# Kernel tuning notes

Hardware: AMD Instinct MI355X
Metric: run time of the kernel (lower is better)

Reference implementation:

```python
import jax, jax.numpy as jnp
import numpy as np

NUM_HEADS = 16
EPS = 1e-6  # LinearAttention.epsilon

def setup_inputs() -> dict:
    key = jax.random.key(0)
    ks = jax.random.split(key, 10)
    B, L, D = 4, 4096, 2048
    s = 1.0 / np.sqrt(D)
    x = jax.random.normal(ks[0], (B, L, D), dtype=jnp.float32)
    attention_mask = jnp.ones((B, L), dtype=jnp.float32)
    Wq = jax.random.normal(ks[1], (D, D), dtype=jnp.float32) * s
    bq = jnp.zeros((D,), dtype=jnp.float32)
    Wk = jax.random.normal(ks[2], (D, D), dtype=jnp.float32) * s
    bk = jnp.zeros((D,), dtype=jnp.float32)
    Wv = jax.random.normal(ks[3], (D, D), dtype=jnp.float32) * s
    bv = jnp.zeros((D,), dtype=jnp.float32)
    Wo = jax.random.normal(ks[4], (D, D), dtype=jnp.float32) * s
    bo = jnp.zeros((D,), dtype=jnp.float32)
    return {"x": x, "attention_mask": attention_mask, "Wq": Wq, "bq": bq,
            "Wk": Wk, "bk": bk, "Wv": Wv, "bv": bv, "Wo": Wo, "bo": bo}

def reference(x, attention_mask, Wq, bq, Wk, bk, Wv, bv, Wo, bo):
    B, L, Dm = x.shape
    H = NUM_HEADS
    Dh = Dm // H
    # q/k/v projections -> [B, H, L, Dh]
    def proj(W, b):
        return (x @ W + b).reshape(B, L, H, Dh).transpose(0, 2, 1, 3)
    q = proj(Wq, bq)
    k = proj(Wk, bk)
    v = proj(Wv, bv)
    # feature map: elu(x) + 1
    q = jax.nn.elu(q) + 1.0
    k = jax.nn.elu(k) + 1.0
    # mask keys/values: mask [B, 1, L, 1]
    m = attention_mask[:, None, :, None]
    k = k * m
    v = v * m
    # causal linear attention via cumulative sums over sequence dim
    k_cum = jnp.cumsum(k, axis=2)          # [B,H,L,Dh]
    kv_cum = jnp.cumsum(k * v, axis=2)     # [B,H,L,Dh] (diagonal kv state, as in source)
    z = jnp.sum(q * k_cum, axis=-1) + EPS  # [B,H,L]
    z = z * attention_mask[:, None, :]
    out = (q * kv_cum) / z[..., None]      # [B,H,L,Dh]
    out = out.transpose(0, 2, 1, 3).reshape(B, L, Dm)
    return out @ Wo + bo
```

## Files before the change

### kernel.cpp

```cpp
#include <hip/hip_runtime.h>
#include <cstdint>
#include <cstddef>

#define EPS_F 1e-6f

__device__ inline unsigned short f2bf(float f) {
    union { float f; unsigned u; } v; v.f = f;
    unsigned r = v.u + 0x7fffu + ((v.u >> 16) & 1u);
    return (unsigned short)(r >> 16);
}
__device__ inline float bf2f(unsigned u16) {
    union { unsigned u; float f; } v; v.u = u16 << 16; return v.f;
}

typedef __attribute__((ext_vector_type(8))) __bf16 bf16x8;
typedef __attribute__((ext_vector_type(8))) short short8;
typedef __attribute__((ext_vector_type(8))) unsigned short ushort8;
typedef __attribute__((ext_vector_type(4))) float floatx4;

__device__ inline void async_load16(const void* g, void* l) {
    __builtin_amdgcn_global_load_lds((const __attribute__((address_space(1))) void*)g,
                                     (__attribute__((address_space(3))) void*)l,
                                     16, 0, 0);
}

__global__ void cast_x_kernel(const float* __restrict__ in, unsigned short* __restrict__ out, int n8) {
    int i = blockIdx.x * blockDim.x + threadIdx.x;
    if (i < n8) {
        float4 a = ((const float4*)in)[2 * i];
        float4 b = ((const float4*)in)[2 * i + 1];
        short8 o;
        o[0] = (short)f2bf(a.x); o[1] = (short)f2bf(a.y);
        o[2] = (short)f2bf(a.z); o[3] = (short)f2bf(a.w);
        o[4] = (short)f2bf(b.x); o[5] = (short)f2bf(b.y);
        o[6] = (short)f2bf(b.z); o[7] = (short)f2bf(b.w);
        ((short8*)out)[i] = o;
    }
}

__global__ void transpose_cast_kernel(const float* __restrict__ W0, const float* __restrict__ W1,
                                      const float* __restrict__ W2, const float* __restrict__ W3,
                                      unsigned short* __restrict__ WtBase, int n) {
    const float* W = (blockIdx.z == 0) ? W0 : (blockIdx.z == 1) ? W1 : (blockIdx.z == 2) ? W2 : W3;
    unsigned short* Wt = WtBase + (size_t)blockIdx.z * n * n;
    __shared__ float tile[32][33];
    int bx = blockIdx.x * 32;
    int by = blockIdx.y * 32;
    int tx = threadIdx.x;
    int ty = threadIdx.y;
    #pragma unroll
    for (int i = 0; i < 32; i += 8)
        tile[ty + i][tx] = W[(size_t)(by + ty + i) * n + bx + tx];
    __syncthreads();
    #pragma unroll
    for (int i = 0; i < 32; i += 8)
        Wt[(size_t)(bx + ty + i) * n + by + tx] = f2bf(tile[tx][ty + i]);
}

#define BMT 128
#define BNT 128
#define BKT 64
#define DMODEL 2048

template<int FINAL>
__global__ __launch_bounds__(256, 2)
void gemm_kernel(const unsigned short* __restrict__ A,
                 const unsigned short* __restrict__ Bt,
                 const float* __restrict__ b0, const float* __restrict__ b1,
                 const float* __restrict__ b2,
                 const float* __restrict__ mask,
                 unsigned short* __restrict__ qo, unsigned short* __restrict__ ko,
                 unsigned short* __restrict__ vo,
                 float* __restrict__ Cf,
                 int M, int K) {
    __shared__ __align__(16) unsigned short As[BMT * BKT];
    __shared__ __align__(16) unsigned short Bs[BNT * BKT];

    const int tid  = threadIdx.x;
    const int wave = tid >> 6;
    const int lane = tid & 63;
    const int m0    = blockIdx.x * BMT;
    const int nglob = blockIdx.y * BNT;
    int mat, n0;
    const float* bias;
    unsigned short* Cb = nullptr;
    if (FINAL) {
        mat = 0; n0 = nglob; bias = b0;
    } else {
        mat  = nglob >> 11;
        n0   = nglob & (DMODEL - 1);
        bias = (mat == 0) ? b0 : (mat == 1) ? b1 : b2;
        Cb   = (mat == 0) ? qo : (mat == 1) ? ko : vo;
    }
    const int wm = (wave >> 1) * 64;
    const int wn = (wave & 1) * 64;
    const int quad  = lane >> 4;
    const int row16 = lane & 15;

    floatx4 acc[4][4] = {};

    const int srow_lo = lane >> 3;
    const int schunk  = lane & 7;

    for (int k0 = 0; k0 < K; k0 += BKT) {
        #pragma unroll
        for (int i = 0; i < 4; i++) {
            int slot_base = wave * 256 + i * 64;
            int r  = wave * 32 + i * 8 + srow_lo;
            int cg = schunk ^ (r & 7);
            const unsigned short* ga = A  + (size_t)(m0 + r) * K + k0 + cg * 8;
            const unsigned short* gb = Bt + (size_t)(nglob + r) * K + k0 + cg * 8;
            async_load16(ga, As + (size_t)slot_base * 8);
            async_load16(gb, Bs + (size_t)slot_base * 8);
        }
        __syncthreads();

        #pragma unroll
        for (int kk = 0; kk < 2; kk++) {
            bf16x8 af[4], bfr[4];
            #pragma unroll
            for (int t = 0; t < 4; t++) {
                int ra = wm + t * 16 + row16;
                int ca = (kk * 4 + quad) ^ (ra & 7);
                af[t]  = __builtin_bit_cast(bf16x8, *(const short8*)(As + (size_t)ra * 64 + ca * 8));
                int rb = wn + t * 16 + row16;
                int cb = (kk * 4 + quad) ^ (rb & 7);
                bfr[t] = __builtin_bit_cast(bf16x8, *(const short8*)(Bs + (size_t)rb * 64 + cb * 8));
            }
            #pragma unroll
            for (int i = 0; i < 4; i++)
                #pragma unroll
                for (int j = 0; j < 4; j++)
                    acc[i][j] = __builtin_amdgcn_mfma_f32_16x16x32_bf16(af[i], bfr[j], acc[i][j], 0, 0, 0);
        }
        __syncthreads();
    }

    float bcache[4];
    #pragma unroll
    for (int j = 0; j < 4; j++) bcache[j] = bias[n0 + wn + j * 16 + row16];
    #pragma unroll
    for (int i = 0; i < 4; i++) {
        #pragma unroll
        for (int r = 0; r < 4; r++) {
            int row = m0 + wm + i * 16 + quad * 4 + r;
            float mr = 1.0f;
            if (!FINAL && mat >= 1) mr = mask[row];
            #pragma unroll
            for (int j = 0; j < 4; j++) {
                int col = n0 + wn + j * 16 + row16;
                float v = acc[i][j][r] + bcache[j];
                if (FINAL) {
                    Cf[(size_t)row * DMODEL + col] = v;
                } else {
                    if (mat <= 1) v = (v > 0.f) ? (v + 1.f) : __expf(v);
                    v *= mr;
                    Cb[(size_t)row * DMODEL + col] = f2bf(v);
                }
            }
        }
    }
}

#define SL    4096
#define SD    2048
#define SH    16
#define CHUNK 64
#define NCH   64

__global__ void scan_partial_kernel(const unsigned short* __restrict__ k,
                                    const unsigned short* __restrict__ v,
                                    float* __restrict__ sumK, float* __restrict__ sumKV) {
    int blk = blockIdx.x;
    int c = blk & (NCH - 1), bh = blk >> 6;
    int b = bh >> 4, h = bh & (SH - 1);
    int lane = threadIdx.x;
    int tg = lane >> 4, dg = lane & 15;
    size_t base = ((size_t)(b * SL + c * CHUNK + tg)) * SD + h * 128 + dg * 8;
    float sk[8] = {0.f, 0.f, 0.f, 0.f, 0.f, 0.f, 0.f, 0.f};
    float skv[8] = {0.f, 0.f, 0.f, 0.f, 0.f, 0.f, 0.f, 0.f};
    for (int it = 0; it < CHUNK / 4; it++) {
        ushort8 kw = *(const ushort8*)(k + base);
        ushort8 vw = *(const ushort8*)(v + base);
        #pragma unroll
        for (int j = 0; j < 8; j++) {
            float kf = bf2f(kw[j]);
            float vf = bf2f(vw[j]);
            sk[j] += kf; skv[j] += kf * vf;
        }
        base += (size_t)4 * SD;
    }
    #pragma unroll
    for (int j = 0; j < 8; j++) {
        sk[j]  += __shfl_xor(sk[j], 16);  sk[j]  += __shfl_xor(sk[j], 32);
        skv[j] += __shfl_xor(skv[j], 16); skv[j] += __shfl_xor(skv[j], 32);
    }
    if (tg == 0) {
        size_t o = ((size_t)bh * NCH + c) * 128 + dg * 8;
        *(float4*)(sumK  + o)     = make_float4(sk[0], sk[1], sk[2], sk[3]);
        *(float4*)(sumK  + o + 4) = make_float4(sk[4], sk[5], sk[6], sk[7]);
        *(float4*)(sumKV + o)     = make_float4(skv[0], skv[1], skv[2], skv[3]);
        *(float4*)(sumKV + o + 4) = make_float4(skv[4], skv[5], skv[6], skv[7]);
    }
}

__global__ void scan_offsets_kernel(const float* __restrict__ sumK, const float* __restrict__ sumKV,
                                    float* __restrict__ offK, float* __restrict__ offKV) {
    int bh = blockIdx.x;
    int d  = threadIdx.x;
    float aK = 0.f, aKV = 0.f;
    for (int c = 0; c < NCH; c++) {
        size_t o = ((size_t)bh * NCH + c) * 128 + d;
        float sk = sumK[o], skv = sumKV[o];
        offK[o] = aK; offKV[o] = aKV;
        aK += sk; aKV += skv;
    }
}

__global__ void scan_final_kernel(const unsigned short* __restrict__ q,
                                  const unsigned short* __restrict__ k,
                                  const unsigned short* __restrict__ v,
                                  const float* __restrict__ offK, const float* __restrict__ offKV,
                                  const float* __restrict__ mask,
                                  unsigned short* __restrict__ out) {
    int blk = blockIdx.x;
    int c = blk & (NCH - 1), bh = blk >> 6;
    int b = bh >> 4, h = bh & (SH - 1);
    int lane = threadIdx.x;
    size_t ob = ((size_t)bh * NCH + c) * 128 + 2 * lane;
    float2 kcv = *(const float2*)(offK  + ob);
    float2 kvv = *(const float2*)(offKV + ob);
    float kc0 = kcv.x, kc1 = kcv.y, kv0 = kvv.x, kv1 = kvv.y;
    size_t base = ((size_t)(b * SL + c * CHUNK)) * SD + h * 128 + 2 * lane;
    const float* mrow = mask + (size_t)b * SL + c * CHUNK;
    for (int s = 0; s < CHUNK / 4; s++) {
        unsigned kw[4], vw[4], qw[4];
        #pragma unroll
        for (int u = 0; u < 4; u++) {
            size_t a = base + (size_t)u * SD;
            kw[u] = *(const unsigned*)(k + a);
            vw[u] = *(const unsigned*)(v + a);
            qw[u] = *(const unsigned*)(q + a);
        }
        float p[4], n0[4], n1[4];
        #pragma unroll
        for (int u = 0; u < 4; u++) {
            float kk0 = bf2f(kw[u] & 0xffff), kk1 = bf2f(kw[u] >> 16);
            float vv0 = bf2f(vw[u] & 0xffff), vv1 = bf2f(vw[u] >> 16);
            float qq0 = bf2f(qw[u] & 0xffff), qq1 = bf2f(qw[u] >> 16);
            kc0 += kk0; kc1 += kk1;
            kv0 += kk0 * vv0; kv1 += kk1 * vv1;
            p[u]  = qq0 * kc0 + qq1 * kc1;
            n0[u] = qq0 * kv0; n1[u] = qq1 * kv1;
        }
        #pragma unroll
        for (int off = 32; off > 0; off >>= 1) {
            #pragma unroll
            for (int u = 0; u < 4; u++) p[u] += __shfl_xor(p[u], off);
        }
        #pragma unroll
        for (int u = 0; u < 4; u++) {
            float z = (p[u] + EPS_F) * mrow[s * 4 + u];
            float inv = 1.0f / z;
            unsigned o0 = f2bf(n0[u] * inv);
            unsigned o1 = f2bf(n1[u] * inv);
            *(unsigned*)(out + base + (size_t)u * SD) = o0 | (o1 << 16);
        }
        base += (size_t)4 * SD;
    }
}

extern "C" void kernel_launch(void* const* d_in, const int* in_sizes, int n_in,
                              void* d_out, int out_size, void* d_ws, size_t ws_size,
                              hipStream_t stream) {
    const float* x  = (const float*)d_in[0];
    const float* am = (const float*)d_in[1];
    const float* Wq = (const float*)d_in[2];
    const float* bq = (const float*)d_in[3];
    const float* Wk = (const float*)d_in[4];
    const float* bk = (const float*)d_in[5];
    const float* Wv = (const float*)d_in[6];
    const float* bv = (const float*)d_in[7];
    const float* Wo = (const float*)d_in[8];
    const float* bo = (const float*)d_in[9];
    float* out = (float*)d_out;

    const int Bb = 4, L = 4096, D = 2048;
    const int M = Bb * L;
    const size_t MD = (size_t)M * D;

    char* w = (char*)d_ws;
    unsigned short* xb    = (unsigned short*)w; w += MD * 2;
    unsigned short* qb    = (unsigned short*)w; w += MD * 2;
    unsigned short* kb    = (unsigned short*)w; w += MD * 2;
    unsigned short* vb    = (unsigned short*)w; w += MD * 2;
    unsigned short* WT    = (unsigned short*)w; w += (size_t)4 * D * D * 2;
    float* sumK  = (float*)w; w += (size_t)64 * NCH * 128 * 4;
    float* sumKV = (float*)w; w += (size_t)64 * NCH * 128 * 4;
    float* offK  = (float*)w; w += (size_t)64 * NCH * 128 * 4;
    float* offKV = (float*)w; w += (size_t)64 * NCH * 128 * 4;
    unsigned short* attnb = xb;

    int n8 = (int)(MD / 8);
    cast_x_kernel<<<(n8 + 255) / 256, 256, 0, stream>>>(x, xb, n8);
    dim3 tb(32, 8);
    dim3 tg(D / 32, D / 32, 4);
    transpose_cast_kernel<<<tg, tb, 0, stream>>>(Wq, Wk, Wv, Wo, WT, D);

    dim3 gq(M / BMT, 3 * D / BNT);
    gemm_kernel<0><<<gq, 256, 0, stream>>>(xb, WT, bq, bk, bv, am, qb, kb, vb, nullptr, M, D);

    scan_partial_kernel<<<64 * NCH, 64, 0, stream>>>(kb, vb, sumK, sumKV);
    scan_offsets_kernel<<<64, 128, 0, stream>>>(sumK, sumKV, offK, offKV);
    scan_final_kernel<<<64 * NCH, 64, 0, stream>>>(qb, kb, vb, offK, offKV, am, attnb);

    dim3 go(M / BMT, D / BNT);
    gemm_kernel<1><<<go, 256, 0, stream>>>(attnb, WT + (size_t)3 * D * D, bo, nullptr, nullptr,
                                           nullptr, nullptr, nullptr, nullptr, out, M, D);
}
```

Baseline: 915.8 us.

## Swizzle GEMM workgroups across XCDs, batch scan offset loads, unroll final scan

Remaps the GEMM block index so consecutive workgroups on the same XCD (bid&7 grouping) cover contiguous tiles, aiming for better L2 reuse on the multi-die GPU. The offsets scan is split into 128 blocks of 64 threads and loads 32 chunk sums into registers before the serial prefix, exposing more memory-level parallelism. The final scan processes 8 rows per iteration instead of 4 to raise loads in flight. This costs more registers, and the swizzle assumes the workgroup count divides by 8.

```diff
diff --git a/kernel.cpp b/kernel.cpp
--- a/kernel.cpp
+++ b/kernel.cpp
@@ -79,8 +79,16 @@
     const int tid  = threadIdx.x;
     const int wave = tid >> 6;
     const int lane = tid & 63;
-    const int m0    = blockIdx.x * BMT;
-    const int nglob = blockIdx.y * BNT;
+
+    const int nwg = (int)(gridDim.x * gridDim.y);
+    const int bid = (int)(blockIdx.y * gridDim.x + blockIdx.x);
+    const int cpx = nwg >> 3;
+    const int swz = (bid & 7) * cpx + (bid >> 3);
+    const int bm  = swz % (int)gridDim.x;
+    const int bn  = swz / (int)gridDim.x;
+
+    const int m0    = bm * BMT;
+    const int nglob = bn * BNT;
     int mat, n0;
     const float* bias;
     unsigned short* Cb = nullptr;
@@ -204,16 +212,27 @@
     }
 }
 
-__global__ void scan_offsets_kernel(const float* __restrict__ sumK, const float* __restrict__ sumKV,
-                                    float* __restrict__ offK, float* __restrict__ offKV) {
-    int bh = blockIdx.x;
-    int d  = threadIdx.x;
+__global__ __launch_bounds__(64)
+void scan_offsets_kernel(const float* __restrict__ sumK, const float* __restrict__ sumKV,
+                         float* __restrict__ offK, float* __restrict__ offKV) {
+    int blk = blockIdx.x;
+    int bh  = blk >> 1;
+    int d   = (blk & 1) * 64 + threadIdx.x;
     float aK = 0.f, aKV = 0.f;
-    for (int c = 0; c < NCH; c++) {
-        size_t o = ((size_t)bh * NCH + c) * 128 + d;
-        float sk = sumK[o], skv = sumKV[o];
-        offK[o] = aK; offKV[o] = aKV;
-        aK += sk; aKV += skv;
+    #pragma unroll 1
+    for (int h = 0; h < 2; h++) {
+        float vK[32], vKV[32];
+        #pragma unroll
+        for (int c2 = 0; c2 < 32; c2++) {
+            size_t o = ((size_t)bh * NCH + h * 32 + c2) * 128 + d;
+            vK[c2] = sumK[o]; vKV[c2] = sumKV[o];
+        }
+        #pragma unroll
+        for (int c2 = 0; c2 < 32; c2++) {
+            size_t o = ((size_t)bh * NCH + h * 32 + c2) * 128 + d;
+            offK[o]  = aK;  aK  += vK[c2];
+            offKV[o] = aKV; aKV += vKV[c2];
+        }
     }
 }
 
@@ -233,18 +252,18 @@
     float kc0 = kcv.x, kc1 = kcv.y, kv0 = kvv.x, kv1 = kvv.y;
     size_t base = ((size_t)(b * SL + c * CHUNK)) * SD + h * 128 + 2 * lane;
     const float* mrow = mask + (size_t)b * SL + c * CHUNK;
-    for (int s = 0; s < CHUNK / 4; s++) {
-        unsigned kw[4], vw[4], qw[4];
-        #pragma unroll
-        for (int u = 0; u < 4; u++) {
+    for (int s = 0; s < CHUNK / 8; s++) {
+        unsigned kw[8], vw[8], qw[8];
+        #pragma unroll
+        for (int u = 0; u < 8; u++) {
             size_t a = base + (size_t)u * SD;
             kw[u] = *(const unsigned*)(k + a);
             vw[u] = *(const unsigned*)(v + a);
             qw[u] = *(const unsigned*)(q + a);
         }
-        float p[4], n0[4], n1[4];
-        #pragma unroll
-        for (int u = 0; u < 4; u++) {
+        float p[8], n0[8], n1[8];
+        #pragma unroll
+        for (int u = 0; u < 8; u++) {
             float kk0 = bf2f(kw[u] & 0xffff), kk1 = bf2f(kw[u] >> 16);
             float vv0 = bf2f(vw[u] & 0xffff), vv1 = bf2f(vw[u] >> 16);
             float qq0 = bf2f(qw[u] & 0xffff), qq1 = bf2f(qw[u] >> 16);
@@ -256,17 +275,17 @@
         #pragma unroll
         for (int off = 32; off > 0; off >>= 1) {
             #pragma unroll
-            for (int u = 0; u < 4; u++) p[u] += __shfl_xor(p[u], off);
-        }
-        #pragma unroll
-        for (int u = 0; u < 4; u++) {
-            float z = (p[u] + EPS_F) * mrow[s * 4 + u];
+            for (int u = 0; u < 8; u++) p[u] += __shfl_xor(p[u], off);
+        }
+        #pragma unroll
+        for (int u = 0; u < 8; u++) {
+            float z = (p[u] + EPS_F) * mrow[s * 8 + u];
             float inv = 1.0f / z;
             unsigned o0 = f2bf(n0[u] * inv);
             unsigned o1 = f2bf(n1[u] * inv);
             *(unsigned*)(out + base + (size_t)u * SD) = o0 | (o1 << 16);
         }
-        base += (size_t)4 * SD;
+        base += (size_t)8 * SD;
     }
 }
 
@@ -311,7 +330,7 @@
     gemm_kernel<0><<<gq, 256, 0, stream>>>(xb, WT, bq, bk, bv, am, qb, kb, vb, nullptr, M, D);
 
     scan_partial_kernel<<<64 * NCH, 64, 0, stream>>>(kb, vb, sumK, sumKV);
-    scan_offsets_kernel<<<64, 128, 0, stream>>>(sumK, sumKV, offK, offKV);
+    scan_offsets_kernel<<<128, 64, 0, stream>>>(sumK, sumKV, offK, offKV);
     scan_final_kernel<<<64 * NCH, 64, 0, stream>>>(qb, kb, vb, offK, offKV, am, attnb);
 
     dim3 go(M / BMT, D / BNT);
```

Measured after the change: 977.5 us. +6.7%, slower.
